# Optimization experiments

Hardware: AMD Instinct MI355X
Metric: run time of the kernel (lower is better)

## Reference

```python
import jax, jax.numpy as jnp
import numpy as np

B, V, N, IN_F, HEADS, OUT_F = 4, 4, 1000, 64, 4, 32
D = HEADS * OUT_F  # 128, concat=True
E = 64000
NEG_SLOPE = 0.2


def setup_inputs() -> dict:
    key = jax.random.key(0)
    ks = jax.random.split(key, 8)
    x = jax.random.normal(ks[0], (B, V, N, IN_F), jnp.float32)
    edge_index = jax.random.randint(ks[1], (2, E), 0, B * N, dtype=jnp.int64)
    W = jax.random.normal(ks[2], (HEADS * OUT_F, IN_F), jnp.float32) / np.sqrt(IN_F)
    att = jax.random.normal(ks[3], (1, HEADS, 2 * OUT_F), jnp.float32) * 0.1
    in_proj_w = jax.random.normal(ks[4], (3 * D, D), jnp.float32) / np.sqrt(D)
    in_proj_b = jnp.zeros((3 * D,), jnp.float32)
    out_proj_w = jax.random.normal(ks[5], (D, D), jnp.float32) / np.sqrt(D)
    out_proj_b = jnp.zeros((D,), jnp.float32)
    bias = jnp.zeros((D,), jnp.float32)
    return dict(x=x, W=W, att=att, in_proj_w=in_proj_w, in_proj_b=in_proj_b,
                out_proj_w=out_proj_w, out_proj_b=out_proj_b, bias=bias,
                edge_index=edge_index)


def reference(x, W, att, in_proj_w, in_proj_b, out_proj_w, out_proj_b, bias, edge_index):
    Bx, Vx, Nx, _ = x.shape
    Ntot = Bx * Nx
    # intra-view GAT: shared W across views
    h = jnp.einsum('bvni,oi->bvno', x, W).reshape(Bx, Vx, Nx, HEADS, OUT_F)
    # block-diagonal placement: h_full[b*V+v, b*N:(b+1)*N] = h[b,v]
    ib = jnp.arange(Bx)
    hf = jnp.zeros((Bx, Vx, Bx, Nx, HEADS, OUT_F), x.dtype).at[ib, :, ib].set(h)
    h_full = hf.reshape(Bx * Vx, Ntot, HEADS, OUT_F)
    # add self loops
    loops = jnp.arange(Ntot, dtype=edge_index.dtype)
    src = jnp.concatenate([edge_index[0], loops])
    dst = jnp.concatenate([edge_index[1], loops])
    # attention scores (faithful to source: flatten h_full over (B*V, Ntot) and
    # index with raw node ids, i.e. gathers from block 0 only)
    h_flat = h_full.reshape(Bx * Vx * Ntot, HEADS, OUT_F)
    h_cat = jnp.concatenate([h_flat[src], h_flat[dst]], axis=-1)  # [Etot, H, 2*OUT]
    att_in = jax.nn.leaky_relu(h_cat, NEG_SLOPE)
    scores = jnp.sum(att * att_in, axis=-1)  # [Etot, HEADS]
    # per-destination segment softmax
    seg_max = jax.ops.segment_max(scores, dst, num_segments=Ntot)
    seg_max = jax.lax.stop_gradient(jnp.where(jnp.isfinite(seg_max), seg_max, 0.0))
    ex = jnp.exp(scores - seg_max[dst])
    denom = jax.ops.segment_sum(ex, dst, num_segments=Ntot)
    alpha = ex / (denom[dst] + 1e-16)  # [Etot, HEADS]
    # scatter-add aggregation, broadcast over B*V rows
    msgs = h_full[:, src] * alpha[None, :, :, None]  # [B*V, Etot, H, OUT]
    out_full = jnp.zeros_like(h_full).at[:, dst].add(msgs)
    # extract each graph's own node block
    out = out_full.reshape(Bx, Vx, Bx, Nx, HEADS, OUT_F)[ib, :, ib]  # [B,V,N,H,OUT]
    h_gat = out.reshape(Bx, Vx, Nx, HEADS * OUT_F)  # concat heads
    # inter-view mixing: MHA over the V axis per node
    seq = h_gat.transpose(0, 2, 1, 3).reshape(Bx * Nx, Vx, D)
    q, k, v = jnp.split(seq @ in_proj_w.T + in_proj_b, 3, axis=-1)
    hd = D // HEADS
    sp = lambda t: t.reshape(Bx * Nx, Vx, HEADS, hd).transpose(0, 2, 1, 3)
    q, k, v = sp(q), sp(k), sp(v)
    aw = jax.nn.softmax(jnp.einsum('bhqd,bhkd->bhqk', q, k) / jnp.sqrt(jnp.asarray(hd, x.dtype)), axis=-1)
    ao = jnp.einsum('bhqk,bhkd->bhqd', aw, v).transpose(0, 2, 1, 3).reshape(Bx * Nx, Vx, D)
    mixed = ao @ out_proj_w.T + out_proj_b
    h_mixed = mixed.reshape(Bx, Nx, Vx, D).transpose(0, 2, 1, 3)  # [B,V,N,D]
    return h_mixed + bias
```

## Files before the change

### kernel.cpp

```cpp
#include <hip/hip_runtime.h>

#define NN 1000
#define HEADS_ 4
#define DM 128
#define EE 64000
#define NTOT 4000
#define ETOT 68000
#define CAP 48
#define EB 34

template <int K, int SCORE, int REMAP>
__device__ void gemm_tile(int mi, int ni,
                          const float* __restrict__ A, const float* __restrict__ Wt,
                          const float* __restrict__ b1, const float* __restrict__ b2,
                          float* __restrict__ C, int N,
                          const float* __restrict__ att,
                          float* __restrict__ ssrc, float* __restrict__ sdst) {
  __shared__ float As[128 * 64];
  __shared__ float Bs[64 * 64];
  int tid = threadIdx.x;
  int m0 = mi * 128, n0 = ni * 64;
  int tx = tid & 15, ty = tid >> 4;
  const float4* A4 = (const float4*)A;
  const float4* W4 = (const float4*)Wt;
  float acc[8][4] = {};

  for (int c = 0; c < K / 64; ++c) {
    __syncthreads();
    {
      int q = tid & 15;
      int r0 = tid >> 4;
#pragma unroll
      for (int p = 0; p < 8; ++p) {
        int r = r0 + p * 16;
        float4 v = A4[(size_t)(m0 + r) * (K / 4) + c * 16 + q];
        *(float4*)&As[r * 64 + ((q ^ ((r >> 2) & 15)) << 2)] = v;
      }
#pragma unroll
      for (int p = 0; p < 4; ++p) {
        int r = r0 + p * 16;
        float4 v = W4[(size_t)(n0 + r) * (K / 4) + c * 16 + q];
        *(float4*)&Bs[r * 64 + ((q ^ ((r >> 2) & 15)) << 2)] = v;
      }
    }
    __syncthreads();
#pragma unroll 4
    for (int q = 0; q < 16; ++q) {
      float4 a[8], b[4];
#pragma unroll
      for (int i = 0; i < 8; ++i) {
        int r = ty * 8 + i;
        a[i] = *(const float4*)&As[r * 64 + ((q ^ ((r >> 2) & 15)) << 2)];
      }
#pragma unroll
      for (int j = 0; j < 4; ++j) {
        int rn = tx * 4 + j;
        b[j] = *(const float4*)&Bs[rn * 64 + ((q ^ ((rn >> 2) & 15)) << 2)];
      }
#pragma unroll
      for (int i = 0; i < 8; ++i)
#pragma unroll
        for (int j = 0; j < 4; ++j)
          acc[i][j] += a[i].x * b[j].x + a[i].y * b[j].y
                     + a[i].z * b[j].z + a[i].w * b[j].w;
    }
  }

  float bd[4] = {0.f, 0.f, 0.f, 0.f};
  int nc = n0 + tx * 4;
  if (b1) { bd[0] = b1[nc]; bd[1] = b1[nc+1]; bd[2] = b1[nc+2]; bd[3] = b1[nc+3]; }
  if (b2) { bd[0] += b2[nc]; bd[1] += b2[nc+1]; bd[2] += b2[nc+2]; bd[3] += b2[nc+3]; }
#pragma unroll
  for (int i = 0; i < 8; ++i) {
    int m = m0 + ty * 8 + i;
    int om = m;
    if (REMAP) {
      int node = m >> 2, v = m & 3;
      int b = node / NN, n = node - b * NN;
      om = (b * 4 + v) * NN + n;
    }
    float4 o = make_float4(acc[i][0] + bd[0], acc[i][1] + bd[1],
                           acc[i][2] + bd[2], acc[i][3] + bd[3]);
    *(float4*)&C[(size_t)om * N + nc] = o;
  }

  if (SCORE && m0 < NN) {
    int hsel = tx >> 3;
    int h = ni * 2 + hsel;
    int kb = (tx & 7) * 4;
    float a0[4], a1[4];
#pragma unroll
    for (int j = 0; j < 4; ++j) {
      a0[j] = att[h * 64 + kb + j];
      a1[j] = att[h * 64 + 32 + kb + j];
    }
#pragma unroll
    for (int i = 0; i < 8; ++i) {
      int m = m0 + ty * 8 + i;
      float p0 = 0.f, p1 = 0.f;
#pragma unroll
      for (int j = 0; j < 4; ++j) {
        float g = acc[i][j];
        float lr = g > 0.f ? g : 0.2f * g;
        p0 += a0[j] * lr;
        p1 += a1[j] * lr;
      }
      p0 += __shfl_xor(p0, 1, 16); p1 += __shfl_xor(p1, 1, 16);
      p0 += __shfl_xor(p0, 2, 16); p1 += __shfl_xor(p1, 2, 16);
      p0 += __shfl_xor(p0, 4, 16); p1 += __shfl_xor(p1, 4, 16);
      if ((tx & 7) == 0 && m < NN) {
        ssrc[m * HEADS_ + h] = p0;
        sdst[m * HEADS_ + h] = p1;
      }
    }
  }
}

__global__ __launch_bounds__(256) void k1_kernel(const float* __restrict__ x,
                                                 const float* __restrict__ W,
                                                 const float* __restrict__ att,
                                                 float* __restrict__ hbuf,
                                                 float* __restrict__ ssrc,
                                                 float* __restrict__ sdst,
                                                 const int* __restrict__ ei,
                                                 int* __restrict__ cnt,
                                                 int* __restrict__ elist) {
  int bid = blockIdx.x;
  if (bid < 250) {
    gemm_tile<64, 1, 0>(bid >> 1, bid & 1, x, W, nullptr, nullptr, hbuf, 128,
                        att, ssrc, sdst);
  } else {
    for (int e = (bid - 250) * 256 + threadIdx.x; e < ETOT; e += EB * 256) {
      int s, d;
      if (e < EE) { s = ei[e]; d = ei[EE + e]; }
      else { s = d = e - EE; }
      int pos = atomicAdd(&cnt[d], 1);
      if (pos < CAP) elist[d * CAP + pos] = s;
    }
  }
}

__global__ __launch_bounds__(256) void gather_kernel(const int* __restrict__ cnt,
                                                     const int* __restrict__ elist,
                                                     const float* __restrict__ ssrc,
                                                     const float* __restrict__ sdst,
                                                     const float* __restrict__ hbuf,
                                                     float* __restrict__ hgat) {
  __shared__ int   srcs[2][CAP];
  __shared__ float exs[2][CAP][HEADS_];
  int li = threadIdx.x >> 7;
  int t = threadIdx.x & 127;
  int d = blockIdx.x * 2 + li;
  int b = d / NN;
  int v = t >> 5, q = t & 31, h = q >> 3;
  int m = cnt[d]; if (m > CAP) m = CAP;
  for (int base = 0; base < m; base += 32) {
    int i = base + (t >> 2);
    if (i < m) {
      int s = elist[d * CAP + i];
      if ((t & 3) == 0) srcs[li][i] = s;
      float sc = ssrc[s * HEADS_ + (t & 3)] + sdst[d * HEADS_ + (t & 3)];
      exs[li][i][t & 3] = __expf(sc);
    }
  }
  __syncthreads();
  float den = 1e-16f;
  float4 acc = make_float4(0.f, 0.f, 0.f, 0.f);
  const float* hbase = hbuf + ((size_t)(b * 4 + v) * NN) * DM + q * 4;
  for (int i = 0; i < m; ++i) {
    float ex = exs[li][i][h];
    den += ex;
    unsigned sl = (unsigned)(srcs[li][i] - b * NN);
    if (sl < NN) {
      float4 hv = *(const float4*)(hbase + (size_t)sl * DM);
      acc.x += ex * hv.x; acc.y += ex * hv.y;
      acc.z += ex * hv.z; acc.w += ex * hv.w;
    }
  }
  float r = 1.f / den;
  acc.x *= r; acc.y *= r; acc.z *= r; acc.w *= r;
  *(float4*)&hgat[((size_t)(d * 4 + v)) * DM + q * 4] = acc;
}

__global__ __launch_bounds__(256) void qkv_kernel(const float* __restrict__ hgat,
                                                  const float* __restrict__ inw,
                                                  const float* __restrict__ inb,
                                                  float* __restrict__ qkv) {
  gemm_tile<128, 0, 0>(blockIdx.x, blockIdx.y, hgat, inw, inb, nullptr, qkv,
                       384, nullptr, nullptr, nullptr);
}

__global__ __launch_bounds__(256) void attn_kernel(const float* __restrict__ qkv,
                                                   float* __restrict__ ao) {
  int li = threadIdx.x >> 7;
  int t = threadIdx.x & 127;
  int node = blockIdx.x * 2 + li;
  __shared__ float qs[2][4][DM], ks[2][4][DM], vs[2][4][DM];
  __shared__ float aw[2][4][HEADS_][4];
#pragma unroll
  for (int v = 0; v < 4; ++v) {
    size_t base = (size_t)(node * 4 + v) * 384;
    qs[li][v][t] = qkv[base + t];
    ks[li][v][t] = qkv[base + 128 + t];
    vs[li][v][t] = qkv[base + 256 + t];
  }
  __syncthreads();
  if (t < 64) {
    int vq = t >> 4, vk = (t >> 2) & 3, h = t & 3;
    float acc = 0.f;
#pragma unroll
    for (int kd = 0; kd < 32; ++kd)
      acc += qs[li][vq][h * 32 + kd] * ks[li][vk][h * 32 + kd];
    aw[li][vq][h][vk] = acc * 0.17677669529663687f;
  }
  __syncthreads();
  if (t < 16) {
    int vq = t >> 2, h = t & 3;
    float mx = aw[li][vq][h][0];
    for (int i = 1; i < 4; ++i) mx = fmaxf(mx, aw[li][vq][h][i]);
    float e[4], s = 0.f;
    for (int i = 0; i < 4; ++i) { e[i] = __expf(aw[li][vq][h][i] - mx); s += e[i]; }
    for (int i = 0; i < 4; ++i) aw[li][vq][h][i] = e[i] / s;
  }
  __syncthreads();
  int h = t >> 5;
#pragma unroll
  for (int vq = 0; vq < 4; ++vq) {
    float acc = 0.f;
#pragma unroll
    for (int vk = 0; vk < 4; ++vk) acc += aw[li][vq][h][vk] * vs[li][vk][t];
    ao[(size_t)(node * 4 + vq) * DM + t] = acc;
  }
}

__global__ __launch_bounds__(256) void outproj_kernel(const float* __restrict__ ao,
                                                      const float* __restrict__ outw,
                                                      const float* __restrict__ outb,
                                                      const float* __restrict__ bias,
                                                      float* __restrict__ out) {
  gemm_tile<128, 0, 1>(blockIdx.x, blockIdx.y, ao, outw, outb, bias, out, 128,
                       nullptr, nullptr, nullptr);
}

extern "C" void kernel_launch(void* const* d_in, const int* in_sizes, int n_in,
                              void* d_out, int out_size, void* d_ws, size_t ws_size,
                              hipStream_t stream) {
  const float* x    = (const float*)d_in[0];
  const float* W    = (const float*)d_in[1];
  const float* att  = (const float*)d_in[2];
  const float* inw  = (const float*)d_in[3];
  const float* inb  = (const float*)d_in[4];
  const float* outw = (const float*)d_in[5];
  const float* outb = (const float*)d_in[6];
  const float* bias = (const float*)d_in[7];
  const int*   ei   = (const int*)d_in[8];
  float* out = (float*)d_out;

  float* ws = (float*)d_ws;
  float* hbuf  = ws;
  float* hgat  = ws + 2100000;
  float* qkv   = ws + 4200000;
  float* ao    = ws + 10400000;
  float* ssrc  = ws + 12500000;
  float* sdst  = ssrc + 16000;
  int*   cnt   = (int*)(sdst + 16000);
  int*   elist = cnt + 4000;

  hipMemsetAsync(ssrc, 0, 36000 * sizeof(float), stream);

  k1_kernel<<<250 + EB, 256, 0, stream>>>(x, W, att, hbuf, ssrc, sdst, ei, cnt, elist);
  gather_kernel<<<NTOT / 2, 256, 0, stream>>>(cnt, elist, ssrc, sdst, hbuf, hgat);
  qkv_kernel<<<dim3(125, 6), 256, 0, stream>>>(hgat, inw, inb, qkv);
  attn_kernel<<<NTOT / 2, 256, 0, stream>>>(qkv, ao);
  outproj_kernel<<<dim3(125, 2), 256, 0, stream>>>(ao, outw, outb, bias, out);
}
```

Baseline: 151.0 us.

## Fuse inter-view attention with output projection into one kernel

Merges the attention kernel and the output-projection GEMM so the attention output stays in shared memory and is multiplied by a shared-memory-staged, skewed copy of out_proj_w within the same block. This removes one kernel launch and the global write and read of the intermediate attention-output buffer. In exchange, each of the 2000 blocks reloads the full 128x128 weight matrix in two halves and uses more shared memory, which may reduce occupancy and add redundant weight traffic.

```diff
diff --git a/kernel.cpp b/kernel.cpp
--- a/kernel.cpp
+++ b/kernel.cpp
@@ -9,10 +9,10 @@
 #define CAP 48
 #define EB 34
 
-template <int K, int SCORE, int REMAP>
+template <int K, int SCORE>
 __device__ void gemm_tile(int mi, int ni,
                           const float* __restrict__ A, const float* __restrict__ Wt,
-                          const float* __restrict__ b1, const float* __restrict__ b2,
+                          const float* __restrict__ b1,
                           float* __restrict__ C, int N,
                           const float* __restrict__ att,
                           float* __restrict__ ssrc, float* __restrict__ sdst) {
@@ -69,19 +69,12 @@
   float bd[4] = {0.f, 0.f, 0.f, 0.f};
   int nc = n0 + tx * 4;
   if (b1) { bd[0] = b1[nc]; bd[1] = b1[nc+1]; bd[2] = b1[nc+2]; bd[3] = b1[nc+3]; }
-  if (b2) { bd[0] += b2[nc]; bd[1] += b2[nc+1]; bd[2] += b2[nc+2]; bd[3] += b2[nc+3]; }
 #pragma unroll
   for (int i = 0; i < 8; ++i) {
     int m = m0 + ty * 8 + i;
-    int om = m;
-    if (REMAP) {
-      int node = m >> 2, v = m & 3;
-      int b = node / NN, n = node - b * NN;
-      om = (b * 4 + v) * NN + n;
-    }
     float4 o = make_float4(acc[i][0] + bd[0], acc[i][1] + bd[1],
                            acc[i][2] + bd[2], acc[i][3] + bd[3]);
-    *(float4*)&C[(size_t)om * N + nc] = o;
+    *(float4*)&C[(size_t)m * N + nc] = o;
   }
 
   if (SCORE && m0 < NN) {
@@ -127,8 +120,7 @@
                                                  int* __restrict__ elist) {
   int bid = blockIdx.x;
   if (bid < 250) {
-    gemm_tile<64, 1, 0>(bid >> 1, bid & 1, x, W, nullptr, nullptr, hbuf, 128,
-                        att, ssrc, sdst);
+    gemm_tile<64, 1>(bid >> 1, bid & 1, x, W, nullptr, hbuf, 128, att, ssrc, sdst);
   } else {
     for (int e = (bid - 250) * 256 + threadIdx.x; e < ETOT; e += EB * 256) {
       int s, d;
@@ -186,17 +178,24 @@
                                                   const float* __restrict__ inw,
                                                   const float* __restrict__ inb,
                                                   float* __restrict__ qkv) {
-  gemm_tile<128, 0, 0>(blockIdx.x, blockIdx.y, hgat, inw, inb, nullptr, qkv,
-                       384, nullptr, nullptr, nullptr);
-}
-
-__global__ __launch_bounds__(256) void attn_kernel(const float* __restrict__ qkv,
-                                                   float* __restrict__ ao) {
-  int li = threadIdx.x >> 7;
-  int t = threadIdx.x & 127;
-  int node = blockIdx.x * 2 + li;
+  gemm_tile<128, 0>(blockIdx.x, blockIdx.y, hgat, inw, inb, qkv, 384,
+                    nullptr, nullptr, nullptr);
+}
+
+__global__ __launch_bounds__(256) void attn_out_kernel(const float* __restrict__ qkv,
+                                                       const float* __restrict__ outw,
+                                                       const float* __restrict__ outb,
+                                                       const float* __restrict__ bias,
+                                                       float* __restrict__ out) {
   __shared__ float qs[2][4][DM], ks[2][4][DM], vs[2][4][DM];
   __shared__ float aw[2][4][HEADS_][4];
+  __shared__ float ao_s[2][4][DM];
+  __shared__ float owt[64 * 128];
+  int tid = threadIdx.x;
+  int li = tid >> 7;
+  int t = tid & 127;
+  int node = blockIdx.x * 2 + li;
+  int b = node / NN, n = node - b * NN;
 #pragma unroll
   for (int v = 0; v < 4; ++v) {
     size_t base = (size_t)(node * 4 + v) * 384;
@@ -223,23 +222,44 @@
     for (int i = 0; i < 4; ++i) aw[li][vq][h][i] = e[i] / s;
   }
   __syncthreads();
-  int h = t >> 5;
-#pragma unroll
-  for (int vq = 0; vq < 4; ++vq) {
-    float acc = 0.f;
-#pragma unroll
-    for (int vk = 0; vk < 4; ++vk) acc += aw[li][vq][h][vk] * vs[li][vk][t];
-    ao[(size_t)(node * 4 + vq) * DM + t] = acc;
-  }
-}
-
-__global__ __launch_bounds__(256) void outproj_kernel(const float* __restrict__ ao,
-                                                      const float* __restrict__ outw,
-                                                      const float* __restrict__ outb,
-                                                      const float* __restrict__ bias,
-                                                      float* __restrict__ out) {
-  gemm_tile<128, 0, 1>(blockIdx.x, blockIdx.y, ao, outw, outb, bias, out, 128,
-                       nullptr, nullptr, nullptr);
+  {
+    int h = t >> 5;
+#pragma unroll
+    for (int vq = 0; vq < 4; ++vq) {
+      float acc = 0.f;
+#pragma unroll
+      for (int vk = 0; vk < 4; ++vk) acc += aw[li][vq][h][vk] * vs[li][vk][t];
+      ao_s[li][vq][t] = acc;
+    }
+  }
+  float accp[4];
+  float base_b = outb[t] + bias[t];
+#pragma unroll
+  for (int vq = 0; vq < 4; ++vq) accp[vq] = base_b;
+  const float4* outw4 = (const float4*)outw;
+  const float4* ao4 = (const float4*)&ao_s[li][0][0];
+  for (int p = 0; p < 2; ++p) {
+    __syncthreads();
+    for (int it = 0; it < 8; ++it) {
+      int idx = tid + it * 256;
+      int j = idx >> 4, k4 = idx & 15;
+      float4 w = outw4[j * 32 + p * 16 + k4];
+      *(float4*)&owt[(j * 16 + ((k4 + j) & 15)) * 4] = w;
+    }
+    __syncthreads();
+#pragma unroll 4
+    for (int k4 = 0; k4 < 16; ++k4) {
+      float4 w = *(const float4*)&owt[(t * 16 + ((k4 + t) & 15)) * 4];
+#pragma unroll
+      for (int vq = 0; vq < 4; ++vq) {
+        float4 a = ao4[vq * 32 + p * 16 + k4];
+        accp[vq] += a.x * w.x + a.y * w.y + a.z * w.z + a.w * w.w;
+      }
+    }
+  }
+#pragma unroll
+  for (int vq = 0; vq < 4; ++vq)
+    out[((size_t)(b * 4 + vq) * NN + n) * DM + t] = accp[vq];
 }
 
 extern "C" void kernel_launch(void* const* d_in, const int* in_sizes, int n_in,
@@ -260,8 +280,7 @@
   float* hbuf  = ws;
   float* hgat  = ws + 2100000;
   float* qkv   = ws + 4200000;
-  float* ao    = ws + 10400000;
-  float* ssrc  = ws + 12500000;
+  float* ssrc  = ws + 10400000;
   float* sdst  = ssrc + 16000;
   int*   cnt   = (int*)(sdst + 16000);
   int*   elist = cnt + 4000;
@@ -271,6 +290,5 @@
   k1_kernel<<<250 + EB, 256, 0, stream>>>(x, W, att, hbuf, ssrc, sdst, ei, cnt, elist);
   gather_kernel<<<NTOT / 2, 256, 0, stream>>>(cnt, elist, ssrc, sdst, hbuf, hgat);
   qkv_kernel<<<dim3(125, 6), 256, 0, stream>>>(hgat, inw, inb, qkv);
-  attn_kernel<<<NTOT / 2, 256, 0, stream>>>(qkv, ao);
-  outproj_kernel<<<dim3(125, 2), 256, 0, stream>>>(ao, outw, outb, bias, out);
-}
+  attn_out_kernel<<<NTOT / 2, 256, 0, stream>>>(qkv, outw, outb, bias, out);
+}
```

Measured after the change: 154.0 us. Within noise of the previous version (+2.0%).
